# Kernel tuning notes

Hardware: AMD Instinct MI355X
Metric: run time of the kernel (lower is better)

## Reference

```python
import jax, jax.numpy as jnp
import numpy as np

B, S, D = 8, 1024, 1024
E, M, K = 8, 4096, 2
GROUP = 1024
CAP = int(np.ceil(GROUP * K / E))  # 256 tokens per expert per group


def setup_inputs() -> dict:
    key = jax.random.key(0)
    ks = jax.random.split(key, 4)
    x = jax.random.normal(ks[0], (B, S, D), dtype=jnp.float32)
    w_router = jax.random.normal(ks[1], (D, E), dtype=jnp.float32) * 0.02
    w1 = jax.random.normal(ks[2], (E, D, M), dtype=jnp.float32) * (1.0 / np.sqrt(D))
    b1 = jnp.zeros((E, M), dtype=jnp.float32)
    w2 = jax.random.normal(ks[3], (E, M, D), dtype=jnp.float32) * (1.0 / np.sqrt(M))
    b2 = jnp.zeros((E, D), dtype=jnp.float32)
    return {"x": x, "w_router": w_router, "w1": w1, "b1": b1, "w2": w2, "b2": b2}


def _moe_forward(x, w_router, w1, b1, w2, b2):
    # Group tokens: [G, GROUP, D]
    xg = x.reshape(-1, GROUP, D)
    G = xg.shape[0]
    # Router: gates over experts per token.
    logits = jnp.einsum('gsd,de->gse', xg, w_router)
    gates = jax.nn.softmax(logits, axis=-1)  # [G, S, E]
    topk_vals, topk_idx = jax.lax.top_k(gates, K)  # [G, S, K]
    oh = jax.nn.one_hot(topk_idx, E, dtype=xg.dtype)  # [G, S, K, E]

    # Position in each expert's buffer: choice-0 of all tokens has priority
    # over choice-1 (standard top-k MoE priority ordering).
    prev = jnp.zeros((G, 1, E), dtype=xg.dtype)
    dispatch = jnp.zeros((G, GROUP, E, CAP), dtype=xg.dtype)
    combine = jnp.zeros((G, GROUP, E, CAP), dtype=xg.dtype)
    for k in range(K):
        ohk = oh[:, :, k, :]                                  # [G, S, E]
        csum = jnp.cumsum(ohk, axis=1) - ohk + prev           # slots used before this token
        pos_k = jnp.sum(csum * ohk, axis=-1)                  # [G, S]
        keep = (pos_k < CAP).astype(xg.dtype)
        pos_oh = jax.nn.one_hot(pos_k, CAP, dtype=xg.dtype)   # [G, S, C]
        d_k = ohk[:, :, :, None] * pos_oh[:, :, None, :] * keep[:, :, None, None]
        dispatch = dispatch + d_k
        combine = combine + topk_vals[:, :, k, None, None] * d_k
        prev = prev + jnp.sum(ohk, axis=1, keepdims=True)

    # Dispatch tokens into per-expert buffers: [E, G, C, D]
    xe = jnp.einsum('gsec,gsd->egcd', dispatch, xg)
    # Per-expert MLP (gelu, approximate=True as in flax Dense MlpBlock).
    h = jax.nn.gelu(jnp.einsum('egcd,edm->egcm', xe, w1) + b1[:, None, None, :])
    ye = jnp.einsum('egcm,emd->egcd', h, w2) + b2[:, None, None, :]
    # Combine back to tokens, weighted by gates.
    out = jnp.einsum('gsec,egcd->gsd', combine, ye)
    out = out.reshape(B, S, D)

    # Importance auxiliary metric (squared coefficient of variation of gate mass).
    imp = jnp.sum(gates, axis=1)  # [G, E]
    aux = jnp.mean((jnp.std(imp, axis=-1) / jnp.mean(imp, axis=-1)) ** 2)
    return out, aux


def reference(x, w_router, w1, b1, w2, b2):
    return _moe_forward(x, w_router, w1, b1, w2, b2)
```

## Files before the change

### kernel.cpp

```cpp
#include <hip/hip_runtime.h>

#define D_DIM 1024
#define E_EXP 8
#define M_DIM 4096
#define N_GRP 8
#define GRP_SZ 1024
#define CAPACITY 256
#define N_TOK (N_GRP * GRP_SZ)
#define SLOT_ROWS (E_EXP * N_GRP * CAPACITY)
#define ROWS_PER_E (N_GRP * CAPACITY)

typedef _Float16 half8_t __attribute__((ext_vector_type(8)));
typedef float f32x4_t __attribute__((ext_vector_type(4)));

__device__ __forceinline__ void async_copy16(void* lds, const void* gptr) {
  __builtin_amdgcn_global_load_lds(
      (__attribute__((address_space(1))) void*)(void*)(const_cast<void*>(gptr)),
      (__attribute__((address_space(3))) void*)lds,
      16, 0, 0);
}

__device__ __forceinline__ float fast_gelu(float v) {
  float w2 = 1.5957691216057308f * (v + 0.044715f * v * v * v);
  float ex = __expf(w2);
  float t = 1.0f - 2.0f * __builtin_amdgcn_rcpf(1.0f + ex);
  return 0.5f * v * (1.0f + t);
}

__global__ __launch_bounds__(256)
void router_kernel(const float* __restrict__ x, const float* __restrict__ wr,
                   float* __restrict__ gates, int* __restrict__ tk_idx,
                   float* __restrict__ tk_val) {
  __shared__ __attribute__((aligned(16))) float wrT[E_EXP * D_DIM];
  const int tid = threadIdx.x;
  for (int i = tid; i < E_EXP * D_DIM; i += 256) {
    int d = i >> 3, e = i & 7;
    wrT[e * D_DIM + d] = wr[i];
  }
  __syncthreads();
  const int wv = tid >> 6, lane = tid & 63;
  const int token = blockIdx.x * 4 + wv;
  const float4* xr = (const float4*)(x + (size_t)token * D_DIM);
  float lg[8] = {0.f, 0.f, 0.f, 0.f, 0.f, 0.f, 0.f, 0.f};
#pragma unroll
  for (int it = 0; it < 4; it++) {
    float4 v = xr[it * 64 + lane];
#pragma unroll
    for (int e = 0; e < 8; e++) {
      float4 w = *(const float4*)&wrT[e * D_DIM + (it * 64 + lane) * 4];
      lg[e] += v.x * w.x + v.y * w.y + v.z * w.z + v.w * w.w;
    }
  }
#pragma unroll
  for (int off = 32; off > 0; off >>= 1) {
#pragma unroll
    for (int e = 0; e < 8; e++) lg[e] += __shfl_xor(lg[e], off, 64);
  }
  if (lane == 0) {
    float mx = lg[0];
#pragma unroll
    for (int e = 1; e < 8; e++) mx = fmaxf(mx, lg[e]);
    float s = 0.f, g[8];
#pragma unroll
    for (int e = 0; e < 8; e++) { g[e] = expf(lg[e] - mx); s += g[e]; }
    float inv = 1.0f / s;
#pragma unroll
    for (int e = 0; e < 8; e++) { g[e] *= inv; gates[(size_t)token * 8 + e] = g[e]; }
    int i0 = 0; float v0 = g[0];
    for (int e = 1; e < 8; e++) if (g[e] > v0) { v0 = g[e]; i0 = e; }
    int i1 = -1; float v1 = -1.f;
    for (int e = 0; e < 8; e++) if (e != i0 && g[e] > v1) { v1 = g[e]; i1 = e; }
    tk_idx[token * 2 + 0] = i0; tk_idx[token * 2 + 1] = i1;
    tk_val[token * 2 + 0] = v0; tk_val[token * 2 + 1] = v1;
  }
}

__global__ void scan_kernel(const int* __restrict__ tk_idx,
                            int* __restrict__ slot_src,
                            int* __restrict__ assign_row) {
  const int g = blockIdx.x;
  const int lane = threadIdx.x;
  const unsigned long long below = (1ull << lane) - 1ull;
  int ev[32];
#pragma unroll
  for (int k = 0; k < 2; k++)
#pragma unroll
    for (int ch = 0; ch < 16; ch++)
      ev[k * 16 + ch] = tk_idx[((size_t)g * GRP_SZ + ch * 64 + lane) * 2 + k];
  int cnt[8] = {0, 0, 0, 0, 0, 0, 0, 0};
#pragma unroll
  for (int k = 0; k < 2; k++) {
#pragma unroll
    for (int ch = 0; ch < 16; ch++) {
      const int s = ch * 64 + lane;
      const int e = ev[k * 16 + ch];
      int pos = 0;
#pragma unroll
      for (int ee = 0; ee < 8; ee++) {
        unsigned long long m = __ballot(e == ee);
        if (e == ee) pos = cnt[ee] + (int)__popcll(m & below);
        cnt[ee] += (int)__popcll(m);
      }
      int row = (pos < CAPACITY) ? ((e * N_GRP + g) * CAPACITY + pos) : -1;
      assign_row[((size_t)g * GRP_SZ + s) * 2 + k] = row;
      if (row >= 0) slot_src[row] = s;
    }
  }
  for (int e = 0; e < 8; e++)
    for (int c = lane; c < CAPACITY; c += 64)
      if (c >= cnt[e]) slot_src[(e * N_GRP + g) * CAPACITY + c] = -1;
}

__global__ __launch_bounds__(256)
void gather_kernel(const float* __restrict__ x, const int* __restrict__ slot_src,
                   _Float16* __restrict__ A1) {
  const int row = blockIdx.x;
  const int g = (row >> 8) & 7;
  const int t = threadIdx.x;
  const int s = slot_src[row];
  float2* dst = (float2*)(A1 + (size_t)row * D_DIM);
  if (s < 0) { dst[t] = make_float2(0.f, 0.f); return; }
  const float4 v = ((const float4*)x)[((size_t)g * GRP_SZ + s) * (D_DIM / 4) + t];
  union { _Float16 h[4]; float2 f2; } u;
  u.h[0] = (_Float16)v.x; u.h[1] = (_Float16)v.y;
  u.h[2] = (_Float16)v.z; u.h[3] = (_Float16)v.w;
  dst[t] = u.f2;
}

__global__ __launch_bounds__(256)
void transpose_to_fp16_kernel(const float* __restrict__ src, _Float16* __restrict__ dst,
                              int R, int C) {
  __shared__ float tile[32][33];
  const int e = blockIdx.z;
  const int c0 = blockIdx.x * 32, r0 = blockIdx.y * 32;
  const float* sp = src + (size_t)e * R * C;
  _Float16* dp = dst + (size_t)e * R * C;
  {
    const int row = threadIdx.x >> 3;
    const int cb = (threadIdx.x & 7) * 4;
    float4 v = *(const float4*)&sp[(size_t)(r0 + row) * C + c0 + cb];
    tile[row][cb + 0] = v.x; tile[row][cb + 1] = v.y;
    tile[row][cb + 2] = v.z; tile[row][cb + 3] = v.w;
  }
  __syncthreads();
  const int cl = threadIdx.x >> 3;
  const int ch = threadIdx.x & 7;
  union { _Float16 h[4]; float2 f2; } u;
#pragma unroll
  for (int k = 0; k < 4; k++) u.h[k] = (_Float16)tile[ch * 4 + k][cl];
  *(float2*)&dp[(size_t)(c0 + cl) * R + r0 + ch * 4] = u.f2;
}

template <int KDIM, int NDIM, int EPI>
__global__ __launch_bounds__(256)
void gemm_bt_kernel(const _Float16* __restrict__ Aall,
                    const _Float16* __restrict__ BTall,
                    const float* __restrict__ biasAll,
                    void* __restrict__ CoutAll) {
  const int e = blockIdx.z;
  const _Float16* A = Aall + (size_t)e * ROWS_PER_E * KDIM;
  const _Float16* BT = BTall + (size_t)e * NDIM * KDIM;
  const float* bias = biasAll + (size_t)e * NDIM;

  constexpr int NYT = NDIM / 128;
  const int yt = blockIdx.x % NYT;
  const int xt = blockIdx.x / NYT;
  const int rowblk = xt * 128;
  const int colblk = yt * 128;

  const int tid = threadIdx.x;
  const int wave = tid >> 6, lane = tid & 63;
  const int wm = (wave & 1) * 64, wn = (wave >> 1) * 64;

  __shared__ __attribute__((aligned(16))) _Float16 smem[2 * 128 * 64];
  _Float16* As = smem;
  _Float16* Bs = smem + 128 * 64;

  f32x4_t acc[4][4] = {};

  const int l_r = lane >> 3, l_c = lane & 7;
  const _Float16* gA[4];
  const _Float16* gB[4];
  _Float16* ldsA[4];
  _Float16* ldsB[4];
#pragma unroll
  for (int i = 0; i < 4; i++) {
    const int rbase = i * 32 + wave * 8;
    const int r = rbase + l_r;
    const int q = l_c ^ (r & 7);
    gA[i] = A + (size_t)(rowblk + r) * KDIM + q * 8;
    gB[i] = BT + (size_t)(colblk + r) * KDIM + q * 8;
    ldsA[i] = &As[rbase * 64];
    ldsB[i] = &Bs[rbase * 64];
  }

  const int quad = lane >> 4;
  const int ln = lane & 15;
  int offA[4], offB[4];
#pragma unroll
  for (int i = 0; i < 4; i++) {
    int m = wm + i * 16 + ln;
    offA[i] = m * 64 + (quad ^ (m & 7)) * 8;
    int n = wn + i * 16 + ln;
    offB[i] = n * 64 + (quad ^ (n & 7)) * 8;
  }

  for (int kt = 0; kt < KDIM; kt += 64) {
    __syncthreads();
#pragma unroll
    for (int i = 0; i < 4; i++) async_copy16(ldsA[i], gA[i] + kt);
#pragma unroll
    for (int i = 0; i < 4; i++) async_copy16(ldsB[i], gB[i] + kt);
    __syncthreads();
#pragma unroll
    for (int h = 0; h < 2; h++) {
      half8_t af[4], bf[4];
#pragma unroll
      for (int i = 0; i < 4; i++) {
        af[i] = *(const half8_t*)&As[offA[i] ^ (h * 32)];
        bf[i] = *(const half8_t*)&Bs[offB[i] ^ (h * 32)];
      }
#pragma unroll
      for (int i = 0; i < 4; i++)
#pragma unroll
        for (int j = 0; j < 4; j++)
          acc[i][j] = __builtin_amdgcn_mfma_f32_16x16x32_f16(af[i], bf[j], acc[i][j], 0, 0, 0);
    }
  }

  if constexpr (EPI == 1) {
    _Float16* C = (_Float16*)CoutAll + (size_t)e * ROWS_PER_E * NDIM;
#pragma unroll
    for (int p = 0; p < 4; p++) {
      __syncthreads();
      const int lr0 = (wave & 1) * 16 + quad * 4;
#pragma unroll
      for (int j = 0; j < 4; j++) {
        const int col = wn + j * 16 + ln;
        const float bcol = bias[colblk + col];
#pragma unroll
        for (int r = 0; r < 4; r++) {
          float v = acc[p][j][r] + bcol;
          smem[(lr0 + r) * 136 + col] = (_Float16)fast_gelu(v);
        }
      }
      __syncthreads();
#pragma unroll
      for (int q = 0; q < 2; q++) {
        const int lrw = q * 16 + (tid >> 4);
        const int chunk = tid & 15;
        const int gr = (lrw >= 16 ? 64 : 0) + p * 16 + (lrw & 15);
        float4 vv = *(const float4*)&smem[lrw * 136 + chunk * 8];
        *(float4*)&C[(size_t)(rowblk + gr) * NDIM + colblk + chunk * 8] = vv;
      }
    }
  } else {
    float* C = (float*)CoutAll + (size_t)e * ROWS_PER_E * NDIM;
    const int colb = colblk + wn + ln;
    const int rowb = rowblk + wm + quad * 4;
#pragma unroll
    for (int j = 0; j < 4; j++) {
      const int col = colb + j * 16;
      const float bcol = bias[col - colblk + colblk];
#pragma unroll
      for (int i = 0; i < 4; i++) {
#pragma unroll
        for (int r = 0; r < 4; r++) {
          const int row = rowb + i * 16 + r;
          C[(size_t)row * NDIM + col] = acc[i][j][r] + bcol;
        }
      }
    }
  }
}

__global__ __launch_bounds__(256)
void combine_kernel(const float* __restrict__ ye, const int* __restrict__ assign_row,
                    const float* __restrict__ tk_val, float* __restrict__ out) {
  const int t = blockIdx.x;
  const int d = threadIdx.x;
  const int r0 = assign_row[t * 2 + 0];
  const int r1 = assign_row[t * 2 + 1];
  const float g0 = tk_val[t * 2 + 0];
  const float g1 = tk_val[t * 2 + 1];
  const float4* y4 = (const float4*)ye;
  float4 v = make_float4(0.f, 0.f, 0.f, 0.f);
  if (r0 >= 0) {
    float4 a = y4[(size_t)r0 * (D_DIM / 4) + d];
    v.x += g0 * a.x; v.y += g0 * a.y; v.z += g0 * a.z; v.w += g0 * a.w;
  }
  if (r1 >= 0) {
    float4 a = y4[(size_t)r1 * (D_DIM / 4) + d];
    v.x += g1 * a.x; v.y += g1 * a.y; v.z += g1 * a.z; v.w += g1 * a.w;
  }
  ((float4*)out)[(size_t)t * (D_DIM / 4) + d] = v;
}

__global__ __launch_bounds__(256)
void aux1_kernel(const float* __restrict__ gates, float* __restrict__ imp) {
  const int g = blockIdx.x >> 3, e = blockIdx.x & 7;
  const int tid = threadIdx.x, lane = tid & 63, wave = tid >> 6;
  float s = 0.f;
  for (int t = tid; t < GRP_SZ; t += 256)
    s += gates[((size_t)g * GRP_SZ + t) * 8 + e];
#pragma unroll
  for (int off = 32; off > 0; off >>= 1) s += __shfl_xor(s, off, 64);
  __shared__ float ws4[4];
  if (lane == 0) ws4[wave] = s;
  __syncthreads();
  if (tid == 0) imp[blockIdx.x] = ws4[0] + ws4[1] + ws4[2] + ws4[3];
}

__global__ void aux2_kernel(const float* __restrict__ imp, float* __restrict__ aux_out) {
  const int t = threadIdx.x;
  __shared__ float cvS[8];
  if (t < 8) {
    float mean = 0.f;
    for (int k = 0; k < 8; k++) mean += imp[t * 8 + k];
    mean *= 0.125f;
    float var = 0.f;
    for (int k = 0; k < 8; k++) { float dd = imp[t * 8 + k] - mean; var += dd * dd; }
    var *= 0.125f;
    cvS[t] = var / (mean * mean);
  }
  __syncthreads();
  if (t == 0) {
    float a = 0.f;
    for (int k = 0; k < 8; k++) a += cvS[k];
    aux_out[0] = a * 0.125f;
  }
}

extern "C" void kernel_launch(void* const* d_in, const int* in_sizes, int n_in,
                              void* d_out, int out_size, void* d_ws, size_t ws_size,
                              hipStream_t stream) {
  const float* x  = (const float*)d_in[0];
  const float* wr = (const float*)d_in[1];
  const float* w1 = (const float*)d_in[2];
  const float* b1 = (const float*)d_in[3];
  const float* w2 = (const float*)d_in[4];
  const float* b2 = (const float*)d_in[5];
  float* out = (float*)d_out;

  char* ws = (char*)d_ws;
  size_t off = 0;
  auto alloc = [&](size_t bytes) -> void* {
    void* p = ws + off;
    off += (bytes + 255) & ~(size_t)255;
    return p;
  };
  float*     gates      = (float*)alloc((size_t)N_TOK * 8 * 4);
  int*       tk_idx     = (int*)  alloc((size_t)N_TOK * 2 * 4);
  float*     tk_val     = (float*)alloc((size_t)N_TOK * 2 * 4);
  int*       assign_row = (int*)  alloc((size_t)N_TOK * 2 * 4);
  int*       slot_src   = (int*)  alloc((size_t)SLOT_ROWS * 4);
  float*     imp        = (float*)alloc(64 * 4);
  _Float16*  A1  = (_Float16*)alloc((size_t)SLOT_ROWS * D_DIM * 2);
  _Float16*  w1t = (_Float16*)alloc((size_t)E_EXP * M_DIM * D_DIM * 2);
  _Float16*  w2t = (_Float16*)alloc((size_t)E_EXP * D_DIM * M_DIM * 2);
  _Float16*  H   = (_Float16*)alloc((size_t)SLOT_ROWS * M_DIM * 2);
  float*     ye  = (float*)   alloc((size_t)SLOT_ROWS * D_DIM * 4);
  if (off > ws_size) return;

  router_kernel<<<N_TOK / 4, 256, 0, stream>>>(x, wr, gates, tk_idx, tk_val);
  scan_kernel<<<N_GRP, 64, 0, stream>>>(tk_idx, slot_src, assign_row);
  gather_kernel<<<SLOT_ROWS, 256, 0, stream>>>(x, slot_src, A1);
  transpose_to_fp16_kernel<<<dim3(M_DIM / 32, D_DIM / 32, E_EXP), 256, 0, stream>>>(w1, w1t, D_DIM, M_DIM);
  transpose_to_fp16_kernel<<<dim3(D_DIM / 32, M_DIM / 32, E_EXP), 256, 0, stream>>>(w2, w2t, M_DIM, D_DIM);
  gemm_bt_kernel<D_DIM, M_DIM, 1><<<dim3((ROWS_PER_E / 128) * (M_DIM / 128), 1, E_EXP), 256, 0, stream>>>(A1, w1t, b1, H);
  gemm_bt_kernel<M_DIM, D_DIM, 2><<<dim3((ROWS_PER_E / 128) * (D_DIM / 128), 1, E_EXP), 256, 0, stream>>>(H, w2t, b2, ye);
  combine_kernel<<<N_TOK, 256, 0, stream>>>(ye, assign_row, tk_val, out);
  aux1_kernel<<<64, 256, 0, stream>>>(gates, imp);
  aux2_kernel<<<1, 64, 0, stream>>>(imp, out + (size_t)N_TOK * D_DIM);
}
```

Baseline: 801.9 us.

## Double-buffer LDS tiles in expert GEMMs and merge weight transpose launches

The GEMM kernel now uses two LDS buffers per operand. The next K-tile's async global-to-LDS copy is issued before computing on the current tile, which removes one barrier per iteration and overlaps the load latency with the MFMA work. This doubles LDS use per block to 64KB, which may reduce how many blocks fit on a CU. Separately, the two weight transpose/fp16 conversion kernels are merged into a single launch to save launch overhead.

```diff
diff --git a/kernel.cpp b/kernel.cpp
--- a/kernel.cpp
+++ b/kernel.cpp
@@ -128,13 +128,17 @@
 }
 
 __global__ __launch_bounds__(256)
-void transpose_to_fp16_kernel(const float* __restrict__ src, _Float16* __restrict__ dst,
-                              int R, int C) {
+void transpose_both_kernel(const float* __restrict__ w1, const float* __restrict__ w2,
+                           _Float16* __restrict__ w1t, _Float16* __restrict__ w2t) {
   __shared__ float tile[32][33];
-  const int e = blockIdx.z;
-  const int c0 = blockIdx.x * 32, r0 = blockIdx.y * 32;
-  const float* sp = src + (size_t)e * R * C;
-  _Float16* dp = dst + (size_t)e * R * C;
+  const int z = blockIdx.y;
+  const float* sp;
+  _Float16* dp;
+  int R, C;
+  if (z < 8) { sp = w1 + (size_t)z * D_DIM * M_DIM; dp = w1t + (size_t)z * D_DIM * M_DIM; R = D_DIM; C = M_DIM; }
+  else       { sp = w2 + (size_t)(z - 8) * M_DIM * D_DIM; dp = w2t + (size_t)(z - 8) * M_DIM * D_DIM; R = M_DIM; C = D_DIM; }
+  const int tiles_x = C >> 5;
+  const int c0 = (blockIdx.x % tiles_x) * 32, r0 = (blockIdx.x / tiles_x) * 32;
   {
     const int row = threadIdx.x >> 3;
     const int cb = (threadIdx.x & 7) * 4;
@@ -172,17 +176,17 @@
   const int wave = tid >> 6, lane = tid & 63;
   const int wm = (wave & 1) * 64, wn = (wave >> 1) * 64;
 
-  __shared__ __attribute__((aligned(16))) _Float16 smem[2 * 128 * 64];
-  _Float16* As = smem;
-  _Float16* Bs = smem + 128 * 64;
+  __shared__ __attribute__((aligned(16))) _Float16 As0[128 * 64];
+  __shared__ __attribute__((aligned(16))) _Float16 As1[128 * 64];
+  __shared__ __attribute__((aligned(16))) _Float16 Bs0[128 * 64];
+  __shared__ __attribute__((aligned(16))) _Float16 Bs1[128 * 64];
 
   f32x4_t acc[4][4] = {};
 
   const int l_r = lane >> 3, l_c = lane & 7;
   const _Float16* gA[4];
   const _Float16* gB[4];
-  _Float16* ldsA[4];
-  _Float16* ldsB[4];
+  int ldsOff[4];
 #pragma unroll
   for (int i = 0; i < 4; i++) {
     const int rbase = i * 32 + wave * 8;
@@ -190,8 +194,7 @@
     const int q = l_c ^ (r & 7);
     gA[i] = A + (size_t)(rowblk + r) * KDIM + q * 8;
     gB[i] = BT + (size_t)(colblk + r) * KDIM + q * 8;
-    ldsA[i] = &As[rbase * 64];
-    ldsB[i] = &Bs[rbase * 64];
+    ldsOff[i] = rbase * 64;
   }
 
   const int quad = lane >> 4;
@@ -205,20 +208,29 @@
     offB[i] = n * 64 + (quad ^ (n & 7)) * 8;
   }
 
+  _Float16* curA = As0; _Float16* nxtA = As1;
+  _Float16* curB = Bs0; _Float16* nxtB = Bs1;
+
+#pragma unroll
+  for (int i = 0; i < 4; i++) async_copy16(curA + ldsOff[i], gA[i]);
+#pragma unroll
+  for (int i = 0; i < 4; i++) async_copy16(curB + ldsOff[i], gB[i]);
+
   for (int kt = 0; kt < KDIM; kt += 64) {
     __syncthreads();
-#pragma unroll
-    for (int i = 0; i < 4; i++) async_copy16(ldsA[i], gA[i] + kt);
-#pragma unroll
-    for (int i = 0; i < 4; i++) async_copy16(ldsB[i], gB[i] + kt);
-    __syncthreads();
+    if (kt + 64 < KDIM) {
+#pragma unroll
+      for (int i = 0; i < 4; i++) async_copy16(nxtA + ldsOff[i], gA[i] + kt + 64);
+#pragma unroll
+      for (int i = 0; i < 4; i++) async_copy16(nxtB + ldsOff[i], gB[i] + kt + 64);
+    }
 #pragma unroll
     for (int h = 0; h < 2; h++) {
       half8_t af[4], bf[4];
 #pragma unroll
       for (int i = 0; i < 4; i++) {
-        af[i] = *(const half8_t*)&As[offA[i] ^ (h * 32)];
-        bf[i] = *(const half8_t*)&Bs[offB[i] ^ (h * 32)];
+        af[i] = *(const half8_t*)&curA[offA[i] ^ (h * 32)];
+        bf[i] = *(const half8_t*)&curB[offB[i] ^ (h * 32)];
       }
 #pragma unroll
       for (int i = 0; i < 4; i++)
@@ -226,6 +238,9 @@
         for (int j = 0; j < 4; j++)
           acc[i][j] = __builtin_amdgcn_mfma_f32_16x16x32_f16(af[i], bf[j], acc[i][j], 0, 0, 0);
     }
+    _Float16* t;
+    t = curA; curA = nxtA; nxtA = t;
+    t = curB; curB = nxtB; nxtB = t;
   }
 
   if constexpr (EPI == 1) {
@@ -241,7 +256,7 @@
 #pragma unroll
         for (int r = 0; r < 4; r++) {
           float v = acc[p][j][r] + bcol;
-          smem[(lr0 + r) * 136 + col] = (_Float16)fast_gelu(v);
+          As0[(lr0 + r) * 136 + col] = (_Float16)fast_gelu(v);
         }
       }
       __syncthreads();
@@ -250,7 +265,7 @@
         const int lrw = q * 16 + (tid >> 4);
         const int chunk = tid & 15;
         const int gr = (lrw >= 16 ? 64 : 0) + p * 16 + (lrw & 15);
-        float4 vv = *(const float4*)&smem[lrw * 136 + chunk * 8];
+        float4 vv = *(const float4*)&As0[lrw * 136 + chunk * 8];
         *(float4*)&C[(size_t)(rowblk + gr) * NDIM + colblk + chunk * 8] = vv;
       }
     }
@@ -261,7 +276,7 @@
 #pragma unroll
     for (int j = 0; j < 4; j++) {
       const int col = colb + j * 16;
-      const float bcol = bias[col - colblk + colblk];
+      const float bcol = bias[col];
 #pragma unroll
       for (int i = 0; i < 4; i++) {
 #pragma unroll
@@ -365,8 +380,7 @@
   router_kernel<<<N_TOK / 4, 256, 0, stream>>>(x, wr, gates, tk_idx, tk_val);
   scan_kernel<<<N_GRP, 64, 0, stream>>>(tk_idx, slot_src, assign_row);
   gather_kernel<<<SLOT_ROWS, 256, 0, stream>>>(x, slot_src, A1);
-  transpose_to_fp16_kernel<<<dim3(M_DIM / 32, D_DIM / 32, E_EXP), 256, 0, stream>>>(w1, w1t, D_DIM, M_DIM);
-  transpose_to_fp16_kernel<<<dim3(D_DIM / 32, M_DIM / 32, E_EXP), 256, 0, stream>>>(w2, w2t, M_DIM, D_DIM);
+  transpose_both_kernel<<<dim3(4096, 16), 256, 0, stream>>>(w1, w2, w1t, w2t);
   gemm_bt_kernel<D_DIM, M_DIM, 1><<<dim3((ROWS_PER_E / 128) * (M_DIM / 128), 1, E_EXP), 256, 0, stream>>>(A1, w1t, b1, H);
   gemm_bt_kernel<M_DIM, D_DIM, 2><<<dim3((ROWS_PER_E / 128) * (D_DIM / 128), 1, E_EXP), 256, 0, stream>>>(H, w2t, b2, ye);
   combine_kernel<<<N_TOK, 256, 0, stream>>>(ye, assign_row, tk_val, out);
```

Result: faster. 749.3 us (-6.6%).
